# Kernel optimization log

Hardware: AMD Instinct MI355X
Metric: run time of the kernel (lower is better)

Reference implementation:

```python
import jax, jax.numpy as jnp
import numpy as np
from jax import lax

NG = 2   # n_groups
NH = 4   # n_heads
LN_EPS = 1e-5

SOBEL_X = np.array([[-1., 0., 1.], [-2., 0., 2.], [-1., 0., 1.]], np.float32)
SOBEL_Y = np.array([[-1., -2., -1.], [0., 0., 0.], [1., 2., 1.]], np.float32)


def conv1x1(x, w, b=None):
    # x: (N, Ci, H, W), w: (Co, Ci)
    y = jnp.einsum('oi,bihw->bohw', w, x)
    if b is not None:
        y = y + b[None, :, None, None]
    return y


def dwconv3(x, w, b=None):
    # depthwise 3x3, stride 1, padding 1. w: (C, 1, 3, 3)
    y = lax.conv_general_dilated(x, w, (1, 1), ((1, 1), (1, 1)),
                                 feature_group_count=x.shape[1],
                                 dimension_numbers=('NCHW', 'OIHW', 'NCHW'))
    if b is not None:
        y = y + b[None, :, None, None]
    return y


def grid_sample_bilinear(img, grid):
    # img: (N, C, H, W); grid: (N, Hg, Wg, 2) with (x, y) in [-1, 1]
    # align_corners=True, zero padding (matches F.grid_sample defaults used here)
    N, C, H, W = img.shape
    gx = (grid[..., 0] + 1.0) * 0.5 * (W - 1)
    gy = (grid[..., 1] + 1.0) * 0.5 * (H - 1)
    x0 = jnp.floor(gx)
    y0 = jnp.floor(gy)
    wx1 = gx - x0
    wy1 = gy - y0

    def gather(yy, xx):
        valid = (yy >= 0) & (yy < H) & (xx >= 0) & (xx < W)
        yc = jnp.clip(yy, 0, H - 1).astype(jnp.int32)
        xc = jnp.clip(xx, 0, W - 1).astype(jnp.int32)
        vals = jax.vmap(lambda im, y_, x_: im[:, y_, x_])(img, yc, xc)  # (N,C,Hg,Wg)
        return vals * valid[:, None, :, :].astype(img.dtype)

    v00 = gather(y0, x0)
    v01 = gather(y0, x0 + 1)
    v10 = gather(y0 + 1, x0)
    v11 = gather(y0 + 1, x0 + 1)
    w00 = ((1 - wy1) * (1 - wx1))[:, None]
    w01 = ((1 - wy1) * wx1)[:, None]
    w10 = (wy1 * (1 - wx1))[:, None]
    w11 = (wy1 * wx1)[:, None]
    return v00 * w00 + v01 * w01 + v10 * w10 + v11 * w11


def setup_inputs() -> dict:
    key = jax.random.key(0)
    B, C, H, W = 4, 128, 48, 48
    Cg = C // NG
    ks = jax.random.split(key, 16)
    s = 0.02
    inp = {
        'x': jax.random.normal(ks[0], (B, C, H, W), jnp.float32),
        'qW': jax.random.normal(ks[1], (C, C), jnp.float32) * s,
        'qb': jnp.zeros((C,), jnp.float32),
        'kW': jax.random.normal(ks[2], (C, C), jnp.float32) * s,
        'kb': jnp.zeros((C,), jnp.float32),
        'vW': jax.random.normal(ks[3], (C, C), jnp.float32) * s,
        'vb': jnp.zeros((C,), jnp.float32),
        'oW': jax.random.normal(ks[4], (C, C), jnp.float32) * s,
        'ob': jnp.zeros((C,), jnp.float32),
        'off_dw_w': jax.random.normal(ks[5], (Cg, 1, 3, 3), jnp.float32) * 0.1,
        'off_dw_b': jnp.zeros((Cg,), jnp.float32),
        'ln_g': jnp.ones((Cg,), jnp.float32),
        'ln_b': jnp.zeros((Cg,), jnp.float32),
        'off_pw_w': jax.random.normal(ks[6], (2, Cg), jnp.float32) * s,
        'sob_w': jax.random.normal(ks[7], (1, Cg), jnp.float32) * 0.1,
        'sob_b': jnp.zeros((1,), jnp.float32),
        'rpe_w': jax.random.normal(ks[8], (C, 1, 3, 3), jnp.float32) * 0.1,
        'rpe_b': jnp.zeros((C,), jnp.float32),
    }
    return inp


def reference(x, qW, qb, kW, kb, vW, vb, oW, ob, off_dw_w, off_dw_b,
              ln_g, ln_b, off_pw_w, sob_w, sob_b, rpe_w, rpe_b):
    B, C, H, W = x.shape
    Cg = C // NG
    Dh = C // NH
    scale = Dh ** -0.5

    q = conv1x1(x, qW, qb)                                   # (B,C,H,W)
    q_off = q.reshape(B * NG, Cg, H, W)                      # (Bg,Cg,H,W)

    # offset branch: dwconv -> LayerNorm(channel) -> GELU -> 1x1 (no bias)
    t = dwconv3(q_off, off_dw_w, off_dw_b)
    tt = t.transpose(0, 2, 3, 1)                             # (Bg,H,W,Cg)
    mu = tt.mean(-1, keepdims=True)
    var = tt.var(-1, keepdims=True)
    tt = (tt - mu) / jnp.sqrt(var + LN_EPS) * ln_g + ln_b
    t = jax.nn.gelu(tt, approximate=False).transpose(0, 3, 1, 2)
    offset = conv1x1(t, off_pw_w)                            # (Bg,2,H,W)

    Hk, Wk = H, W
    n_sample = Hk * Wk
    off_range = jnp.array([1.0 / (Hk - 1.0), 1.0 / (Wk - 1.0)], x.dtype).reshape(1, 2, 1, 1)
    offset = jnp.tanh(offset) * off_range                    # offset_range_factor = 1
    offset = offset.transpose(0, 2, 3, 1)                    # (Bg,Hk,Wk,2)  (y,x)

    # reference points, normalized to [-1,1]
    ref_y = (jnp.linspace(0.5, Hk - 0.5, Hk, dtype=x.dtype) / (Hk - 1.0)) * 2.0 - 1.0
    ref_x = (jnp.linspace(0.5, Wk - 0.5, Wk, dtype=x.dtype) / (Wk - 1.0)) * 2.0 - 1.0
    ref = jnp.stack(jnp.meshgrid(ref_y, ref_x, indexing='ij'), axis=-1)  # (Hk,Wk,2)
    reference = jnp.broadcast_to(ref[None], (B * NG, Hk, Wk, 2))

    # Sobel gate on 1x1-projected q_off
    s = conv1x1(q_off, sob_w, sob_b)                         # (Bg,1,H,W)
    kx = jnp.asarray(SOBEL_X).reshape(1, 1, 3, 3)
    ky = jnp.asarray(SOBEL_Y).reshape(1, 1, 3, 3)
    gxm = dwconv3(s, kx)
    gym = dwconv3(s, ky)
    mag = jnp.sqrt(gxm ** 2 + gym ** 2)
    binary = (mag > 0.5).astype(x.dtype).transpose(0, 2, 3, 1)  # (Bg,H,W,1)

    pos = offset + reference * binary                        # (Bg,Hk,Wk,2) (y,x)

    xs = grid_sample_bilinear(x.reshape(B * NG, Cg, H, W), pos[..., ::-1])  # grid in (x,y)
    xs = xs.reshape(B, C, 1, n_sample)

    qf = q.reshape(B * NH, Dh, H * W)
    k = conv1x1(xs, kW, kb).reshape(B * NH, Dh, n_sample)
    v = conv1x1(xs, vW, vb).reshape(B * NH, Dh, n_sample)

    attn = jnp.einsum('bcm,bcn->bmn', qf, k) * scale         # (B*NH, HW, n_sample)
    lepe = dwconv3(q.reshape(B, C, H, W), rpe_w, rpe_b).reshape(B * NH, Dh, H * W)
    attn = jax.nn.softmax(attn, axis=2)                      # attn_drop: eval identity
    out = jnp.einsum('bmn,bcn->bcm', attn, v) + lepe
    out = out.reshape(B, C, H, W)
    y = conv1x1(out, oW, ob)                                 # proj_drop: eval identity
    return (y, pos, reference)
```

## Files before the change

### kernel.cpp

```cpp
#include <hip/hip_runtime.h>
#include <hip/hip_bf16.h>
#include <math.h>

#define B_   4
#define C_   128
#define H_   48
#define W_   48
#define HW_  2304
#define CG_  64
#define DH_  32
#define NZ_  6
#define SCALE_ 0.17677669529663687f
#define QS_    (0.17677669529663687f * 1.4426950408889634f)
#define INVQ_  (1.0f / QS_)

#define Y_OFF   0
#define POS_OFF 1179648
#define REF_OFF 1216512

#define OFF_XTBF  0
#define OFF_QBF   589824
#define OFF_KBF   1179648
#define OFF_VBF   1769472
#define OFF_XST   2359296
#define OFF_WBF   2949120
#define OFF_PRS   2981888
#define OFF_PROH  3203072
#define OFF_SMAPD 6742016
#define OFF_WEFF  6778880

typedef __attribute__((ext_vector_type(8))) short short8;
typedef __attribute__((ext_vector_type(4))) float f32x4;
typedef __attribute__((ext_vector_type(4))) _Float16 f16x4;
typedef __attribute__((ext_vector_type(8))) _Float16 f16x8;

__device__ inline unsigned short f2bf(float f) {
  unsigned u = __float_as_uint(f);
  u += 0x7fff + ((u >> 16) & 1);
  return (unsigned short)(u >> 16);
}
__device__ inline float bf2f(unsigned short s) {
  return __uint_as_float(((unsigned)s) << 16);
}

__device__ inline short8 pack8(const f32x4 a, const f32x4 b) {
  union { unsigned u[4]; short8 s; } r;
  asm("v_cvt_pk_bf16_f32 %0, %1, %2" : "=v"(r.u[0]) : "v"(a[0]), "v"(a[1]));
  asm("v_cvt_pk_bf16_f32 %0, %1, %2" : "=v"(r.u[1]) : "v"(a[2]), "v"(a[3]));
  asm("v_cvt_pk_bf16_f32 %0, %1, %2" : "=v"(r.u[2]) : "v"(b[0]), "v"(b[1]));
  asm("v_cvt_pk_bf16_f32 %0, %1, %2" : "=v"(r.u[3]) : "v"(b[2]), "v"(b[3]));
  return r.s;
}

__global__ __launch_bounds__(256) void k_pre(const float* __restrict__ x,
                                             const float* __restrict__ qW, const float* __restrict__ kW,
                                             const float* __restrict__ vW, const float* __restrict__ oW,
                                             const float* __restrict__ qb,
                                             const float* __restrict__ sob_w, const float* __restrict__ sob_b,
                                             unsigned short* __restrict__ xTbf,
                                             unsigned short* __restrict__ wbf,
                                             double* __restrict__ weff) {
  int bx = blockIdx.x;
  if (bx < 288) {
    __shared__ float tile[64][65];
    int p0 = (bx % 36) * 64, c0 = ((bx / 36) & 1) * 64, b = bx / 72;
    for (int idx = threadIdx.x; idx < 4096; idx += 256) {
      int cr = idx >> 6, pc = idx & 63;
      tile[cr][pc] = x[((size_t)(b * C_) + c0 + cr) * HW_ + p0 + pc];
    }
    __syncthreads();
    for (int idx = threadIdx.x; idx < 4096; idx += 256) {
      int pr = idx >> 6, cc = idx & 63;
      xTbf[((size_t)(b * HW_) + p0 + pr) * C_ + c0 + cc] = f2bf(tile[cc][pr]);
    }
  } else if (bx < 544) {
    int t = (bx - 288) * 256 + threadIdx.x;
    int which = t >> 14, i = t & 16383;
    const float* src = which == 0 ? qW : which == 1 ? kW : which == 2 ? vW : oW;
    wbf[t] = f2bf(src[i]);
  } else {
    int t = threadIdx.x;
    int g = t >> 7, i = t & 127;
    double acc = 0.0;
    for (int c = 0; c < 64; c++)
      acc += (double)sob_w[c] * (double)qW[(size_t)(g * 64 + c) * C_ + i];
    weff[t] = acc;
    if (t < 2) {
      double bb = (double)sob_b[0];
      for (int c = 0; c < 64; c++) bb += (double)sob_w[c] * (double)qb[t * 64 + c];
      weff[256 + t] = bb;
    }
  }
}

__global__ __launch_bounds__(256, 4) void k_qconv_smapd(const unsigned short* __restrict__ xTbf,
                                                        const unsigned short* __restrict__ wbf,
                                                        const float* __restrict__ qb,
                                                        const float* __restrict__ x,
                                                        const double* __restrict__ weff,
                                                        unsigned short* __restrict__ qbf,
                                                        double* __restrict__ smapd) {
  int bx = blockIdx.x;
  if (bx < 576) {
    int t = threadIdx.x, w = t >> 6, l = t & 63, lg = l >> 4, lo = l & 15;
    int m0 = (bx % 144) * 16, b = bx / 144, o0 = w * 32;
    const unsigned short* xrow = xTbf + ((size_t)(b * HW_) + m0 + lo) * C_ + lg * 8;
    f32x4 acc[2] = {{0.f,0.f,0.f,0.f},{0.f,0.f,0.f,0.f}};
#pragma unroll
    for (int kb = 0; kb < 4; kb++) {
      short8 xf = *(const short8*)(xrow + kb * 32);
#pragma unroll
      for (int os = 0; os < 2; os++) {
        short8 wf = *(const short8*)(wbf + (size_t)(o0 + os * 16 + lo) * C_ + kb * 32 + lg * 8);
        acc[os] = __builtin_amdgcn_mfma_f32_16x16x32_bf16(xf, wf, acc[os], 0, 0, 0);
      }
    }
#pragma unroll
    for (int os = 0; os < 2; os++) {
      int o = o0 + os * 16 + lo;
      float bi = qb[o];
#pragma unroll
      for (int r = 0; r < 4; r++) {
        int m = m0 + lg * 4 + r;
        qbf[((size_t)(b * HW_) + m) * C_ + o] = f2bf((acc[os][r] + bi) * QS_);
      }
    }
  } else {
    int bb = bx - 576;
    int p = (bb % 9) * 256 + threadIdx.x;
    int bg = bb / 9;
    int b = bg >> 1, g = bg & 1;
    const float* xb = x + (size_t)b * C_ * HW_ + p;
    const double* wv = weff + g * 128;
    double acc = weff[256 + g];
#pragma unroll 8
    for (int i = 0; i < 128; i++) acc += wv[i] * (double)xb[(size_t)i * HW_];
    smapd[bg * HW_ + p] = acc;
  }
}

__global__ __launch_bounds__(256) void k_offpos_sample(const unsigned short* __restrict__ qbf,
                                                       const double* __restrict__ s_map,
                                                       const float* __restrict__ dw_w,
                                                       const float* __restrict__ dw_b,
                                                       const float* __restrict__ ln_g,
                                                       const float* __restrict__ ln_b,
                                                       const float* __restrict__ pw_w,
                                                       const unsigned short* __restrict__ xTbf,
                                                       float* __restrict__ out,
                                                       unsigned short* __restrict__ xsT) {
  int widx = blockIdx.x * 4 + (threadIdx.x >> 6);
  int lane = threadIdx.x & 63;
  int bg = widx / HW_;
  int p = widx - bg * HW_;
  int h = p / W_, w = p - h * W_;
  int b = bg >> 1, g = bg & 1;
  const unsigned short* qc = qbf + (size_t)(b * HW_) * C_ + g * 64 + lane;
  float tv = dw_b[lane];
#pragma unroll
  for (int dy = -1; dy <= 1; dy++)
#pragma unroll
    for (int dx = -1; dx <= 1; dx++) {
      int hh = h + dy, ww = w + dx;
      if (hh >= 0 && hh < H_ && ww >= 0 && ww < W_) {
        float wgt = dw_w[lane * 9 + (dy + 1) * 3 + (dx + 1)] * INVQ_;
        tv += wgt * bf2f(qc[(size_t)(hh * W_ + ww) * C_]);
      }
    }
  float ssum = tv, ssq = tv * tv;
#pragma unroll
  for (int msk = 32; msk; msk >>= 1) {
    ssum += __shfl_xor(ssum, msk, 64);
    ssq  += __shfl_xor(ssq,  msk, 64);
  }
  float mu  = ssum * (1.0f / 64.0f);
  float var = ssq * (1.0f / 64.0f) - mu * mu;
  float uu  = (tv - mu) * rsqrtf(var + 1e-5f) * ln_g[lane] + ln_b[lane];
  float gl = 0.5f * uu * (1.0f + erff(uu * 0.70710678118654752f));
  float p0 = pw_w[lane] * gl, p1 = pw_w[64 + lane] * gl;
#pragma unroll
  for (int msk = 32; msk; msk >>= 1) {
    p0 += __shfl_xor(p0, msk, 64);
    p1 += __shfl_xor(p1, msk, 64);
  }
  const double sobx[9] = {-1., 0., 1., -2., 0., 2., -1., 0., 1.};
  const double soby[9] = {-1., -2., -1., 0., 0., 0., 1., 2., 1.};
  float off_y = tanhf(p0) * (1.0f / 47.0f);
  float off_x = tanhf(p1) * (1.0f / 47.0f);
  const double* sm = s_map + bg * HW_;
  double gx = 0., gy = 0.;
#pragma unroll
  for (int dy = -1; dy <= 1; dy++)
#pragma unroll
    for (int dx = -1; dx <= 1; dx++) {
      int hh = h + dy, ww = w + dx;
      if (hh >= 0 && hh < H_ && ww >= 0 && ww < W_) {
        double sv = sm[hh * W_ + ww];
        gx += sobx[(dy + 1) * 3 + dx + 1] * sv;
        gy += soby[(dy + 1) * 3 + dx + 1] * sv;
      }
    }
  double mag = sqrt(gx * gx + gy * gy);
  float bin = mag > 0.5 ? 1.0f : 0.0f;
  float ry = ((h + 0.5f) / 47.0f) * 2.0f - 1.0f;
  float rx = ((w + 0.5f) / 47.0f) * 2.0f - 1.0f;
  float py = off_y + ry * bin;
  float px = off_x + rx * bin;
  if (lane == 0) {
    int pi = (bg * HW_ + p) * 2;
    out[POS_OFF + pi]     = py;
    out[POS_OFF + pi + 1] = px;
    out[REF_OFF + pi]     = ry;
    out[REF_OFF + pi + 1] = rx;
  }
  float gxf = (px + 1.0f) * 0.5f * 47.0f;
  float gyf = (py + 1.0f) * 0.5f * 47.0f;
  float x0 = floorf(gxf), y0 = floorf(gyf);
  float wx1 = gxf - x0, wy1 = gyf - y0;
  float wx0 = 1.0f - wx1, wy0 = 1.0f - wy1;
  const unsigned short* base = xTbf + (size_t)(b * HW_) * C_ + g * 64 + lane;
  float acc = 0.0f;
#pragma unroll
  for (int cy = 0; cy < 2; cy++)
#pragma unroll
    for (int cx = 0; cx < 2; cx++) {
      float yy = y0 + (float)cy, xx = x0 + (float)cx;
      bool valid = (yy >= 0.f) && (yy < 48.f) && (xx >= 0.f) && (xx < 48.f);
      int yc = min(max((int)yy, 0), 47);
      int xc = min(max((int)xx, 0), 47);
      float wgt = (cy ? wy1 : wy0) * (cx ? wx1 : wx0);
      float vv = valid ? bf2f(base[(size_t)(yc * 48 + xc) * C_]) : 0.0f;
      acc += wgt * vv;
    }
  xsT[((size_t)(b * HW_) + p) * C_ + g * 64 + lane] = f2bf(acc);
}

__global__ __launch_bounds__(256, 4) void k_kvconv(const unsigned short* __restrict__ xsT,
                                                   const unsigned short* __restrict__ wbf,
                                                   const float* __restrict__ kbias,
                                                   const float* __restrict__ vbias,
                                                   unsigned short* __restrict__ kbf,
                                                   unsigned short* __restrict__ vbf) {
  int t = threadIdx.x, w = t >> 6, l = t & 63, lg = l >> 4, lo = l & 15;
  int n0 = blockIdx.x * 16, b = blockIdx.y, o0 = w * 32;
  const unsigned short* xrow = xsT + ((size_t)(b * HW_) + n0 + lo) * C_ + lg * 8;
  const unsigned short* wk = wbf + 16384;
  const unsigned short* wv = wbf + 32768;
  f32x4 ak[2] = {{0.f,0.f,0.f,0.f},{0.f,0.f,0.f,0.f}};
  f32x4 av[2] = {{0.f,0.f,0.f,0.f},{0.f,0.f,0.f,0.f}};
#pragma unroll
  for (int kb = 0; kb < 4; kb++) {
    short8 xf = *(const short8*)(xrow + kb * 32);
#pragma unroll
    for (int os = 0; os < 2; os++) {
      size_t wo = (size_t)(o0 + os * 16 + lo) * C_ + kb * 32 + lg * 8;
      short8 wkf = *(const short8*)(wk + wo);
      short8 wvf = *(const short8*)(wv + wo);
      ak[os] = __builtin_amdgcn_mfma_f32_16x16x32_bf16(xf, wkf, ak[os], 0, 0, 0);
      av[os] = __builtin_amdgcn_mfma_f32_16x16x32_bf16(wvf, xf, av[os], 0, 0, 0);
    }
  }
  int o32 = (n0 & 16) + lo;
  int vpos = (n0 & ~31) + ((o32 & 12) << 1) + (o32 & 3) + ((o32 >> 4) << 2);
#pragma unroll
  for (int os = 0; os < 2; os++) {
    int ok = o0 + os * 16 + lo;
    float bk_ = kbias[ok];
#pragma unroll
    for (int r = 0; r < 4; r++) {
      int n = n0 + lg * 4 + r;
      kbf[((size_t)(b * HW_) + n) * C_ + ok] = f2bf(ak[os][r] + bk_);
      int ov = o0 + os * 16 + lg * 4 + r;
      vbf[((size_t)(b * C_) + ov) * HW_ + vpos] = f2bf(av[os][r] + vbias[ov]);
    }
  }
}

#define EXPROW(SV, RS)                                                              \
  _Pragma("unroll")                                                                 \
  for (int r = 0; r < 4; r++) {                                                     \
    float e0, e1, e2, e3;                                                           \
    asm("v_exp_f32 %0, %1" : "=v"(e0) : "v"(SV##0[r]));                             \
    asm("v_exp_f32 %0, %1" : "=v"(e1) : "v"(SV##1[r]));                             \
    asm("v_exp_f32 %0, %1" : "=v"(e2) : "v"(SV##2[r]));                             \
    asm("v_exp_f32 %0, %1" : "=v"(e3) : "v"(SV##3[r]));                             \
    SV##0[r] = e0; SV##1[r] = e1; SV##2[r] = e2; SV##3[r] = e3;                     \
    RS += (e0 + e1) + (e2 + e3);                                                    \
  }

#define ATTN_BODY7(BK, BV, BKN, BVN, DOPREF)                                        \
  {                                                                                 \
    if (DOPREF) {                                                                   \
      _Pragma("unroll")                                                             \
      for (int sub = 0; sub < 4; sub++)                                             \
        BKN[sub] = *(const short8*)(kb_ + (size_t)(n0 + 64 + sub * 16 + lo) * C_);  \
      BVN[0] = *(const short8*)(vr0 + n0 + 64);                                     \
      BVN[1] = *(const short8*)(vr0 + n0 + 96);                                     \
      BVN[2] = *(const short8*)(vr1 + n0 + 64);                                     \
      BVN[3] = *(const short8*)(vr1 + n0 + 96);                                     \
    }                                                                               \
    f32x4 z = {0.f, 0.f, 0.f, 0.f};                                                 \
    __builtin_amdgcn_s_setprio(1);                                                  \
    f32x4 s0 = __builtin_amdgcn_mfma_f32_16x16x32_bf16(BK[0], aq0, z, 0, 0, 0);     \
    f32x4 s1 = __builtin_amdgcn_mfma_f32_16x16x32_bf16(BK[1], aq0, z, 0, 0, 0);     \
    f32x4 s2 = __builtin_amdgcn_mfma_f32_16x16x32_bf16(BK[2], aq0, z, 0, 0, 0);     \
    f32x4 s3 = __builtin_amdgcn_mfma_f32_16x16x32_bf16(BK[3], aq0, z, 0, 0, 0);     \
    __builtin_amdgcn_s_setprio(0);                                                  \
    EXPROW(s, rsum0)                                                                \
    short8 pa0 = pack8(s0, s1), pa1 = pack8(s2, s3);                                \
    __builtin_amdgcn_s_setprio(1);                                                  \
    f32x4 t0 = __builtin_amdgcn_mfma_f32_16x16x32_bf16(BK[0], aq1, z, 0, 0, 0);     \
    f32x4 t1 = __builtin_amdgcn_mfma_f32_16x16x32_bf16(BK[1], aq1, z, 0, 0, 0);     \
    f32x4 t2 = __builtin_amdgcn_mfma_f32_16x16x32_bf16(BK[2], aq1, z, 0, 0, 0);     \
    f32x4 t3 = __builtin_amdgcn_mfma_f32_16x16x32_bf16(BK[3], aq1, z, 0, 0, 0);     \
    acc00 = __builtin_amdgcn_mfma_f32_16x16x32_bf16(pa0, BV[0], acc00, 0, 0, 0);    \
    acc00 = __builtin_amdgcn_mfma_f32_16x16x32_bf16(pa1, BV[1], acc00, 0, 0, 0);    \
    acc01 = __builtin_amdgcn_mfma_f32_16x16x32_bf16(pa0, BV[2], acc01, 0, 0, 0);    \
    acc01 = __builtin_amdgcn_mfma_f32_16x16x32_bf16(pa1, BV[3], acc01, 0, 0, 0);    \
    __builtin_amdgcn_s_setprio(0);                                                  \
    EXPROW(t, rsum1)                                                                \
    short8 pb0 = pack8(t0, t1), pb1 = pack8(t2, t3);                                \
    __builtin_amdgcn_s_setprio(1);                                                  \
    acc10 = __builtin_amdgcn_mfma_f32_16x16x32_bf16(pb0, BV[0], acc10, 0, 0, 0);    \
    acc10 = __builtin_amdgcn_mfma_f32_16x16x32_bf16(pb1, BV[1], acc10, 0, 0, 0);    \
    acc11 = __builtin_amdgcn_mfma_f32_16x16x32_bf16(pb0, BV[2], acc11, 0, 0, 0);    \
    acc11 = __builtin_amdgcn_mfma_f32_16x16x32_bf16(pb1, BV[3], acc11, 0, 0, 0);    \
    __builtin_amdgcn_s_setprio(0);                                                  \
    n0 += 64;                                                                       \
  }

__global__ __launch_bounds__(256, 3) void k_attn7(const unsigned short* __restrict__ qbf,
                                                  const unsigned short* __restrict__ kbf,
                                                  const unsigned short* __restrict__ vpf,
                                                  _Float16* __restrict__ prOh,
                                                  float* __restrict__ prS) {
  int t = threadIdx.x, w = t >> 6, l = t & 63, lg = l >> 4, lo = l & 15;
  int bh = blockIdx.y, b = bh >> 2, hd = bh & 3, nz = blockIdx.z;
  int cb = hd * 32;
  int m0 = blockIdx.x * 128 + w * 32;
  const unsigned short* qrow = qbf + ((size_t)(b * HW_) + m0 + lo) * C_ + cb + lg * 8;
  short8 aq0 = *(const short8*)qrow;
  short8 aq1 = *(const short8*)(qrow + (size_t)16 * C_);
  const unsigned short* kb_ = kbf + (size_t)(b * HW_) * C_ + cb + lg * 8;
  const unsigned short* vr0 = vpf + (size_t)(b * C_ + cb + lo) * HW_ + lg * 8;
  const unsigned short* vr1 = vr0 + (size_t)16 * HW_;
  f32x4 acc00 = {0.f,0.f,0.f,0.f}, acc01 = {0.f,0.f,0.f,0.f};
  f32x4 acc10 = {0.f,0.f,0.f,0.f}, acc11 = {0.f,0.f,0.f,0.f};
  float rsum0 = 0.f, rsum1 = 0.f;
  int n0 = nz * 384;
  short8 bkA[4], bkB[4], bvA[4], bvB[4];
#pragma unroll
  for (int sub = 0; sub < 4; sub++)
    bkA[sub] = *(const short8*)(kb_ + (size_t)(n0 + sub * 16 + lo) * C_);
  bvA[0] = *(const short8*)(vr0 + n0);
  bvA[1] = *(const short8*)(vr0 + n0 + 32);
  bvA[2] = *(const short8*)(vr1 + n0);
  bvA[3] = *(const short8*)(vr1 + n0 + 32);
  for (int i3 = 0; i3 < 3; i3++) {
    ATTN_BODY7(bkA, bvA, bkB, bvB, true)
    ATTN_BODY7(bkB, bvB, bkA, bvA, (i3 < 2))
  }
  rsum0 += __shfl_xor(rsum0, 16, 64);
  rsum0 += __shfl_xor(rsum0, 32, 64);
  rsum1 += __shfl_xor(rsum1, 16, 64);
  rsum1 += __shfl_xor(rsum1, 32, 64);
  _Float16* pr = prOh + (size_t)nz * (B_ * HW_ * C_);
#pragma unroll
  for (int r = 0; r < 4; r++) {
    int m = m0 + lg * 4 + r;
    size_t oi = ((size_t)(b * HW_) + m) * C_ + cb;
    pr[oi + lo] = (_Float16)acc00[r];
    pr[oi + 16 + lo] = (_Float16)acc01[r];
    size_t oi2 = oi + (size_t)16 * C_;
    pr[oi2 + lo] = (_Float16)acc10[r];
    pr[oi2 + 16 + lo] = (_Float16)acc11[r];
  }
  if (l < 16) {
    prS[((size_t)(nz * 16) + bh) * HW_ + m0 + lo] = rsum0;
    prS[((size_t)(nz * 16) + bh) * HW_ + m0 + 16 + lo] = rsum1;
  }
}

__global__ __launch_bounds__(256) void k_out(const _Float16* __restrict__ prOh,
                                             const float* __restrict__ prS,
                                             const unsigned short* __restrict__ qbf,
                                             const float* __restrict__ rpe_w,
                                             const float* __restrict__ rpe_b,
                                             const unsigned short* __restrict__ wbf,
                                             const float* __restrict__ ob_,
                                             float* __restrict__ y) {
  __shared__ __align__(16) unsigned short lds[16][136];
  int t = threadIdx.x;
  int m0 = blockIdx.x * 16, b = blockIdx.y;
  {
    int mi = t >> 4, c8 = (t & 15) * 8;
    int m = m0 + mi;
    int hd = c8 >> 5;
    size_t oi = ((size_t)(b * HW_) + m) * C_ + c8;
    float rs = 0.f;
    float o[8] = {0.f,0.f,0.f,0.f,0.f,0.f,0.f,0.f};
#pragma unroll
    for (int nz = 0; nz < NZ_; nz++) {
      rs += prS[((size_t)(nz * 16) + b * 4 + hd) * HW_ + m];
      f16x8 v = *(const f16x8*)(prOh + (size_t)nz * (B_ * HW_ * C_) + oi);
#pragma unroll
      for (int j = 0; j < 8; j++) o[j] += (float)v[j];
    }
    float inv = 1.0f / rs;
    int h = m / W_, ww0 = m - h * W_;
    float lp[8];
#pragma unroll
    for (int j = 0; j < 8; j++) lp[j] = rpe_b[c8 + j];
#pragma unroll
    for (int dy = -1; dy <= 1; dy++)
#pragma unroll
      for (int dx = -1; dx <= 1; dx++) {
        int hh = h + dy, ww = ww0 + dx;
        if (hh >= 0 && hh < H_ && ww >= 0 && ww < W_) {
          int idx = (dy + 1) * 3 + (dx + 1);
          short8 q8 = *(const short8*)(qbf + ((size_t)(b * HW_) + hh * W_ + ww) * C_ + c8);
#pragma unroll
          for (int j = 0; j < 8; j++)
            lp[j] += rpe_w[(c8 + j) * 9 + idx] * INVQ_ * bf2f((unsigned short)q8[j]);
        }
      }
    short8 res;
#pragma unroll
    for (int j = 0; j < 8; j++) res[j] = (short)f2bf(o[j] * inv + lp[j]);
    *(short8*)&lds[mi][c8] = res;
  }
  __syncthreads();
  int w = t >> 6, l = t & 63, lg = l >> 4, lo = l & 15;
  int o0 = w * 32;
  const unsigned short* wo = wbf + 49152;
  f32x4 acc[2] = {{0.f,0.f,0.f,0.f},{0.f,0.f,0.f,0.f}};
#pragma unroll
  for (int kb = 0; kb < 4; kb++) {
    short8 xf = *(const short8*)&lds[lo][kb * 32 + lg * 8];
#pragma unroll
    for (int os = 0; os < 2; os++) {
      short8 wf = *(const short8*)(wo + (size_t)(o0 + os * 16 + lo) * C_ + kb * 32 + lg * 8);
      acc[os] = __builtin_amdgcn_mfma_f32_16x16x32_bf16(wf, xf, acc[os], 0, 0, 0);
    }
  }
#pragma unroll
  for (int os = 0; os < 2; os++)
#pragma unroll
    for (int r = 0; r < 4; r++) {
      int o = o0 + os * 16 + lg * 4 + r;
      y[((size_t)(b * C_) + o) * HW_ + m0 + lo] = acc[os][r] + ob_[o];
    }
}

extern "C" void kernel_launch(void* const* d_in, const int* in_sizes, int n_in,
                              void* d_out, int out_size, void* d_ws, size_t ws_size,
                              hipStream_t stream) {
  const float* x        = (const float*)d_in[0];
  const float* qW       = (const float*)d_in[1];
  const float* qb       = (const float*)d_in[2];
  const float* kW       = (const float*)d_in[3];
  const float* kb       = (const float*)d_in[4];
  const float* vW       = (const float*)d_in[5];
  const float* vb       = (const float*)d_in[6];
  const float* oW       = (const float*)d_in[7];
  const float* ob       = (const float*)d_in[8];
  const float* off_dw_w = (const float*)d_in[9];
  const float* off_dw_b = (const float*)d_in[10];
  const float* ln_g     = (const float*)d_in[11];
  const float* ln_b     = (const float*)d_in[12];
  const float* off_pw_w = (const float*)d_in[13];
  const float* sob_w    = (const float*)d_in[14];
  const float* sob_b    = (const float*)d_in[15];
  const float* rpe_w    = (const float*)d_in[16];
  const float* rpe_b    = (const float*)d_in[17];
  float* out = (float*)d_out;
  float* wsf = (float*)d_ws;
  unsigned short* xTbf  = (unsigned short*)(wsf + OFF_XTBF);
  unsigned short* qbf   = (unsigned short*)(wsf + OFF_QBF);
  unsigned short* kbf   = (unsigned short*)(wsf + OFF_KBF);
  unsigned short* vbf   = (unsigned short*)(wsf + OFF_VBF);
  unsigned short* xsT   = (unsigned short*)(wsf + OFF_XST);
  unsigned short* wbf   = (unsigned short*)(wsf + OFF_WBF);
  float* prS   = wsf + OFF_PRS;
  _Float16* prOh = (_Float16*)(wsf + OFF_PROH);
  double* smapd = (double*)(wsf + OFF_SMAPD);
  double* weff  = (double*)(wsf + OFF_WEFF);

  k_pre          <<<545,             256, 0, stream>>>(x, qW, kW, vW, oW, qb, sob_w, sob_b,
                                                       xTbf, wbf, weff);
  k_qconv_smapd  <<<648,             256, 0, stream>>>(xTbf, wbf, qb, x, weff, qbf, smapd);
  k_offpos_sample<<<4608,            256, 0, stream>>>(qbf, smapd, off_dw_w, off_dw_b,
                                                       ln_g, ln_b, off_pw_w, xTbf, out, xsT);
  k_kvconv       <<<dim3(144, 4),    256, 0, stream>>>(xsT, wbf, kb, vb, kbf, vbf);
  k_attn7        <<<dim3(18, 16, 6), 256, 0, stream>>>(qbf, kbf, vbf, prOh, prS);
  k_out          <<<dim3(144, 4),    256, 0, stream>>>(prOh, prS, qbf, rpe_w, rpe_b,
                                                       wbf, ob, out + Y_OFF);
}
```

Before: 134.7 us.

## Merge pre-processing and q-conv kernels, cut attention key splits to four

```diff
diff --git a/kernel.cpp b/kernel.cpp
--- a/kernel.cpp
+++ b/kernel.cpp
@@ -9,7 +9,7 @@
 #define HW_  2304
 #define CG_  64
 #define DH_  32
-#define NZ_  6
+#define NZ_  4
 #define SCALE_ 0.17677669529663687f
 #define QS_    (0.17677669529663687f * 1.4426950408889634f)
 #define INVQ_  (1.0f / QS_)
@@ -25,13 +25,11 @@
 #define OFF_XST   2359296
 #define OFF_WBF   2949120
 #define OFF_PRS   2981888
-#define OFF_PROH  3203072
-#define OFF_SMAPD 6742016
-#define OFF_WEFF  6778880
+#define OFF_PROH  4161536
+#define OFF_SMAPD 7184384
 
 typedef __attribute__((ext_vector_type(8))) short short8;
 typedef __attribute__((ext_vector_type(4))) float f32x4;
-typedef __attribute__((ext_vector_type(4))) _Float16 f16x4;
 typedef __attribute__((ext_vector_type(8))) _Float16 f16x8;
 
 __device__ inline unsigned short f2bf(float f) {
@@ -52,66 +50,56 @@
   return r.s;
 }
 
-__global__ __launch_bounds__(256) void k_pre(const float* __restrict__ x,
-                                             const float* __restrict__ qW, const float* __restrict__ kW,
-                                             const float* __restrict__ vW, const float* __restrict__ oW,
-                                             const float* __restrict__ qb,
-                                             const float* __restrict__ sob_w, const float* __restrict__ sob_b,
-                                             unsigned short* __restrict__ xTbf,
-                                             unsigned short* __restrict__ wbf,
-                                             double* __restrict__ weff) {
+__global__ __launch_bounds__(256) void k_front(const float* __restrict__ x,
+                                               const float* __restrict__ qW, const float* __restrict__ kW,
+                                               const float* __restrict__ vW, const float* __restrict__ oW,
+                                               const float* __restrict__ qb,
+                                               const float* __restrict__ sob_w, const float* __restrict__ sob_b,
+                                               unsigned short* __restrict__ xTbf,
+                                               unsigned short* __restrict__ wbf,
+                                               unsigned short* __restrict__ qbf,
+                                               double* __restrict__ smapd) {
+  __shared__ __align__(16) float tile[64][65];
   int bx = blockIdx.x;
+  int t = threadIdx.x;
   if (bx < 288) {
-    __shared__ float tile[64][65];
     int p0 = (bx % 36) * 64, c0 = ((bx / 36) & 1) * 64, b = bx / 72;
-    for (int idx = threadIdx.x; idx < 4096; idx += 256) {
+    for (int idx = t; idx < 4096; idx += 256) {
       int cr = idx >> 6, pc = idx & 63;
       tile[cr][pc] = x[((size_t)(b * C_) + c0 + cr) * HW_ + p0 + pc];
     }
     __syncthreads();
-    for (int idx = threadIdx.x; idx < 4096; idx += 256) {
+    for (int idx = t; idx < 4096; idx += 256) {
       int pr = idx >> 6, cc = idx & 63;
       xTbf[((size_t)(b * HW_) + p0 + pr) * C_ + c0 + cc] = f2bf(tile[cc][pr]);
     }
-  } else if (bx < 544) {
-    int t = (bx - 288) * 256 + threadIdx.x;
-    int which = t >> 14, i = t & 16383;
-    const float* src = which == 0 ? qW : which == 1 ? kW : which == 2 ? vW : oW;
-    wbf[t] = f2bf(src[i]);
-  } else {
-    int t = threadIdx.x;
-    int g = t >> 7, i = t & 127;
-    double acc = 0.0;
-    for (int c = 0; c < 64; c++)
-      acc += (double)sob_w[c] * (double)qW[(size_t)(g * 64 + c) * C_ + i];
-    weff[t] = acc;
-    if (t < 2) {
-      double bb = (double)sob_b[0];
-      for (int c = 0; c < 64; c++) bb += (double)sob_w[c] * (double)qb[t * 64 + c];
-      weff[256 + t] = bb;
-    }
-  }
-}
-
-__global__ __launch_bounds__(256, 4) void k_qconv_smapd(const unsigned short* __restrict__ xTbf,
-                                                        const unsigned short* __restrict__ wbf,
-                                                        const float* __restrict__ qb,
-                                                        const float* __restrict__ x,
-                                                        const double* __restrict__ weff,
-                                                        unsigned short* __restrict__ qbf,
-                                                        double* __restrict__ smapd) {
-  int bx = blockIdx.x;
-  if (bx < 576) {
-    int t = threadIdx.x, w = t >> 6, l = t & 63, lg = l >> 4, lo = l & 15;
-    int m0 = (bx % 144) * 16, b = bx / 144, o0 = w * 32;
-    const unsigned short* xrow = xTbf + ((size_t)(b * HW_) + m0 + lo) * C_ + lg * 8;
+  } else if (bx < 864) {
+    int bb = bx - 288;
+    int m0 = (bb % 144) * 16, b = bb / 144;
+    unsigned short (*xls)[136] = (unsigned short(*)[136])tile;
+#pragma unroll
+    for (int it = 0; it < 2; it++) {
+      int r = it * 64 + (t >> 2);
+      int quad = t & 3;
+      float4 v = *(const float4*)&x[((size_t)(b * C_) + r) * HW_ + m0 + quad * 4];
+      xls[quad * 4 + 0][r] = f2bf(v.x);
+      xls[quad * 4 + 1][r] = f2bf(v.y);
+      xls[quad * 4 + 2][r] = f2bf(v.z);
+      xls[quad * 4 + 3][r] = f2bf(v.w);
+    }
+    __syncthreads();
+    int w = t >> 6, l = t & 63, lg = l >> 4, lo = l & 15;
+    int o0 = w * 32;
     f32x4 acc[2] = {{0.f,0.f,0.f,0.f},{0.f,0.f,0.f,0.f}};
 #pragma unroll
     for (int kb = 0; kb < 4; kb++) {
-      short8 xf = *(const short8*)(xrow + kb * 32);
+      short8 xf = *(const short8*)&xls[lo][kb * 32 + lg * 8];
 #pragma unroll
       for (int os = 0; os < 2; os++) {
-        short8 wf = *(const short8*)(wbf + (size_t)(o0 + os * 16 + lo) * C_ + kb * 32 + lg * 8);
+        const float* wrow = qW + (size_t)(o0 + os * 16 + lo) * C_ + kb * 32 + lg * 8;
+        f32x4 wa = *(const f32x4*)wrow;
+        f32x4 wb = *(const f32x4*)(wrow + 4);
+        short8 wf = pack8(wa, wb);
         acc[os] = __builtin_amdgcn_mfma_f32_16x16x32_bf16(xf, wf, acc[os], 0, 0, 0);
       }
     }
@@ -125,17 +113,33 @@
         qbf[((size_t)(b * HW_) + m) * C_ + o] = f2bf((acc[os][r] + bi) * QS_);
       }
     }
+  } else if (bx < 936) {
+    int bb = bx - 864;
+    int bg = bb / 9, pgrp = bb % 9;
+    int b = bg >> 1, g = bg & 1;
+    __shared__ double wl[129];
+    if (t < 128) {
+      double a = 0.0;
+      for (int c = 0; c < 64; c++)
+        a += (double)sob_w[c] * (double)qW[(size_t)(g * 64 + c) * C_ + t];
+      wl[t] = a;
+    } else if (t == 128) {
+      double bb2 = (double)sob_b[0];
+      for (int c = 0; c < 64; c++) bb2 += (double)sob_w[c] * (double)qb[g * 64 + c];
+      wl[128] = bb2;
+    }
+    __syncthreads();
+    int p = pgrp * 256 + t;
+    const float* xb = x + (size_t)b * C_ * HW_ + p;
+    double acc = wl[128];
+#pragma unroll 8
+    for (int i = 0; i < 128; i++) acc += wl[i] * (double)xb[(size_t)i * HW_];
+    smapd[bg * HW_ + p] = acc;
   } else {
-    int bb = bx - 576;
-    int p = (bb % 9) * 256 + threadIdx.x;
-    int bg = bb / 9;
-    int b = bg >> 1, g = bg & 1;
-    const float* xb = x + (size_t)b * C_ * HW_ + p;
-    const double* wv = weff + g * 128;
-    double acc = weff[256 + g];
-#pragma unroll 8
-    for (int i = 0; i < 128; i++) acc += wv[i] * (double)xb[(size_t)i * HW_];
-    smapd[bg * HW_ + p] = acc;
+    int tt = (bx - 936) * 256 + t;
+    int which = tt >> 14, i = tt & 16383;
+    const float* src = which == 0 ? qW : which == 1 ? kW : which == 2 ? vW : oW;
+    wbf[tt] = f2bf(src[i]);
   }
 }
 
@@ -288,16 +292,16 @@
     RS += (e0 + e1) + (e2 + e3);                                                    \
   }
 
-#define ATTN_BODY7(BK, BV, BKN, BVN, DOPREF)                                        \
+#define ATTN_BODY5(BK, BKN, DOPREF)                                                 \
   {                                                                                 \
+    short8 bv0 = *(const short8*)(vr0 + n0);                                        \
+    short8 bv1 = *(const short8*)(vr0 + n0 + 32);                                   \
+    short8 bv2 = *(const short8*)(vr1 + n0);                                        \
+    short8 bv3 = *(const short8*)(vr1 + n0 + 32);                                   \
     if (DOPREF) {                                                                   \
       _Pragma("unroll")                                                             \
       for (int sub = 0; sub < 4; sub++)                                             \
         BKN[sub] = *(const short8*)(kb_ + (size_t)(n0 + 64 + sub * 16 + lo) * C_);  \
-      BVN[0] = *(const short8*)(vr0 + n0 + 64);                                     \
-      BVN[1] = *(const short8*)(vr0 + n0 + 96);                                     \
-      BVN[2] = *(const short8*)(vr1 + n0 + 64);                                     \
-      BVN[3] = *(const short8*)(vr1 + n0 + 96);                                     \
     }                                                                               \
     f32x4 z = {0.f, 0.f, 0.f, 0.f};                                                 \
     __builtin_amdgcn_s_setprio(1);                                                  \
@@ -313,23 +317,23 @@
     f32x4 t1 = __builtin_amdgcn_mfma_f32_16x16x32_bf16(BK[1], aq1, z, 0, 0, 0);     \
     f32x4 t2 = __builtin_amdgcn_mfma_f32_16x16x32_bf16(BK[2], aq1, z, 0, 0, 0);     \
     f32x4 t3 = __builtin_amdgcn_mfma_f32_16x16x32_bf16(BK[3], aq1, z, 0, 0, 0);     \
-    acc00 = __builtin_amdgcn_mfma_f32_16x16x32_bf16(pa0, BV[0], acc00, 0, 0, 0);    \
-    acc00 = __builtin_amdgcn_mfma_f32_16x16x32_bf16(pa1, BV[1], acc00, 0, 0, 0);    \
-    acc01 = __builtin_amdgcn_mfma_f32_16x16x32_bf16(pa0, BV[2], acc01, 0, 0, 0);    \
-    acc01 = __builtin_amdgcn_mfma_f32_16x16x32_bf16(pa1, BV[3], acc01, 0, 0, 0);    \
+    acc00 = __builtin_amdgcn_mfma_f32_16x16x32_bf16(pa0, bv0, acc00, 0, 0, 0);      \
+    acc00 = __builtin_amdgcn_mfma_f32_16x16x32_bf16(pa1, bv1, acc00, 0, 0, 0);      \
+    acc01 = __builtin_amdgcn_mfma_f32_16x16x32_bf16(pa0, bv2, acc01, 0, 0, 0);      \
+    acc01 = __builtin_amdgcn_mfma_f32_16x16x32_bf16(pa1, bv3, acc01, 0, 0, 0);      \
     __builtin_amdgcn_s_setprio(0);                                                  \
     EXPROW(t, rsum1)                                                                \
     short8 pb0 = pack8(t0, t1), pb1 = pack8(t2, t3);                                \
     __builtin_amdgcn_s_setprio(1);                                                  \
-    acc10 = __builtin_amdgcn_mfma_f32_16x16x32_bf16(pb0, BV[0], acc10, 0, 0, 0);    \
-    acc10 = __builtin_amdgcn_mfma_f32_16x16x32_bf16(pb1, BV[1], acc10, 0, 0, 0);    \
-    acc11 = __builtin_amdgcn_mfma_f32_16x16x32_bf16(pb0, BV[2], acc11, 0, 0, 0);    \
-    acc11 = __builtin_amdgcn_mfma_f32_16x16x32_bf16(pb1, BV[3], acc11, 0, 0, 0);    \
+    acc10 = __builtin_amdgcn_mfma_f32_16x16x32_bf16(pb0, bv0, acc10, 0, 0, 0);      \
+    acc10 = __builtin_amdgcn_mfma_f32_16x16x32_bf16(pb1, bv1, acc10, 0, 0, 0);      \
+    acc11 = __builtin_amdgcn_mfma_f32_16x16x32_bf16(pb0, bv2, acc11, 0, 0, 0);      \
+    acc11 = __builtin_amdgcn_mfma_f32_16x16x32_bf16(pb1, bv3, acc11, 0, 0, 0);      \
     __builtin_amdgcn_s_setprio(0);                                                  \
     n0 += 64;                                                                       \
   }
 
-__global__ __launch_bounds__(256, 3) void k_attn7(const unsigned short* __restrict__ qbf,
+__global__ __launch_bounds__(256, 3) void k_attn8(const unsigned short* __restrict__ qbf,
                                                   const unsigned short* __restrict__ kbf,
                                                   const unsigned short* __restrict__ vpf,
                                                   _Float16* __restrict__ prOh,
@@ -347,19 +351,16 @@
   f32x4 acc00 = {0.f,0.f,0.f,0.f}, acc01 = {0.f,0.f,0.f,0.f};
   f32x4 acc10 = {0.f,0.f,0.f,0.f}, acc11 = {0.f,0.f,0.f,0.f};
   float rsum0 = 0.f, rsum1 = 0.f;
-  int n0 = nz * 384;
-  short8 bkA[4], bkB[4], bvA[4], bvB[4];
+  int n0 = nz * 576;
+  short8 bkA[4], bkB[4];
 #pragma unroll
   for (int sub = 0; sub < 4; sub++)
     bkA[sub] = *(const short8*)(kb_ + (size_t)(n0 + sub * 16 + lo) * C_);
-  bvA[0] = *(const short8*)(vr0 + n0);
-  bvA[1] = *(const short8*)(vr0 + n0 + 32);
-  bvA[2] = *(const short8*)(vr1 + n0);
-  bvA[3] = *(const short8*)(vr1 + n0 + 32);
-  for (int i3 = 0; i3 < 3; i3++) {
-    ATTN_BODY7(bkA, bvA, bkB, bvB, true)
-    ATTN_BODY7(bkB, bvB, bkA, bvA, (i3 < 2))
-  }
+  for (int i4 = 0; i4 < 4; i4++) {
+    ATTN_BODY5(bkA, bkB, true)
+    ATTN_BODY5(bkB, bkA, (i4 < 3))
+  }
+  ATTN_BODY5(bkA, bkB, false)
   rsum0 += __shfl_xor(rsum0, 16, 64);
   rsum0 += __shfl_xor(rsum0, 32, 64);
   rsum1 += __shfl_xor(rsum1, 16, 64);
@@ -484,15 +485,13 @@
   float* prS   = wsf + OFF_PRS;
   _Float16* prOh = (_Float16*)(wsf + OFF_PROH);
   double* smapd = (double*)(wsf + OFF_SMAPD);
-  double* weff  = (double*)(wsf + OFF_WEFF);
-
-  k_pre          <<<545,             256, 0, stream>>>(x, qW, kW, vW, oW, qb, sob_w, sob_b,
-                                                       xTbf, wbf, weff);
-  k_qconv_smapd  <<<648,             256, 0, stream>>>(xTbf, wbf, qb, x, weff, qbf, smapd);
+
+  k_front        <<<1192,            256, 0, stream>>>(x, qW, kW, vW, oW, qb, sob_w, sob_b,
+                                                       xTbf, wbf, qbf, smapd);
   k_offpos_sample<<<4608,            256, 0, stream>>>(qbf, smapd, off_dw_w, off_dw_b,
                                                        ln_g, ln_b, off_pw_w, xTbf, out, xsT);
   k_kvconv       <<<dim3(144, 4),    256, 0, stream>>>(xsT, wbf, kb, vb, kbf, vbf);
-  k_attn7        <<<dim3(18, 16, 6), 256, 0, stream>>>(qbf, kbf, vbf, prOh, prS);
+  k_attn8        <<<dim3(18, 16, 4), 256, 0, stream>>>(qbf, kbf, vbf, prOh, prS);
   k_out          <<<dim3(144, 4),    256, 0, stream>>>(prOh, prS, qbf, rpe_w, rpe_b,
                                                        wbf, ob, out + Y_OFF);
 }
```

After: 130.6 us. -3.0%, faster.

## Reshape attention split: fewer key splits, smaller blocks, drop V prefetch

Applied to the files above, without the earlier changes.

```diff
diff --git a/kernel.cpp b/kernel.cpp
--- a/kernel.cpp
+++ b/kernel.cpp
@@ -9,7 +9,7 @@
 #define HW_  2304
 #define CG_  64
 #define DH_  32
-#define NZ_  6
+#define NZ_  4
 #define SCALE_ 0.17677669529663687f
 #define QS_    (0.17677669529663687f * 1.4426950408889634f)
 #define INVQ_  (1.0f / QS_)
@@ -25,13 +25,12 @@
 #define OFF_XST   2359296
 #define OFF_WBF   2949120
 #define OFF_PRS   2981888
-#define OFF_PROH  3203072
-#define OFF_SMAPD 6742016
-#define OFF_WEFF  6778880
+#define OFF_PROH  4161536
+#define OFF_SMAPD 7184384
+#define OFF_WEFF  7221248
 
 typedef __attribute__((ext_vector_type(8))) short short8;
 typedef __attribute__((ext_vector_type(4))) float f32x4;
-typedef __attribute__((ext_vector_type(4))) _Float16 f16x4;
 typedef __attribute__((ext_vector_type(8))) _Float16 f16x8;
 
 __device__ inline unsigned short f2bf(float f) {
@@ -288,16 +287,16 @@
     RS += (e0 + e1) + (e2 + e3);                                                    \
   }
 
-#define ATTN_BODY7(BK, BV, BKN, BVN, DOPREF)                                        \
+#define ATTN_BODY5(BK, BKN, DOPREF)                                                 \
   {                                                                                 \
+    short8 bv0 = *(const short8*)(vr0 + n0);                                        \
+    short8 bv1 = *(const short8*)(vr0 + n0 + 32);                                   \
+    short8 bv2 = *(const short8*)(vr1 + n0);                                        \
+    short8 bv3 = *(const short8*)(vr1 + n0 + 32);                                   \
     if (DOPREF) {                                                                   \
       _Pragma("unroll")                                                             \
       for (int sub = 0; sub < 4; sub++)                                             \
         BKN[sub] = *(const short8*)(kb_ + (size_t)(n0 + 64 + sub * 16 + lo) * C_);  \
-      BVN[0] = *(const short8*)(vr0 + n0 + 64);                                     \
-      BVN[1] = *(const short8*)(vr0 + n0 + 96);                                     \
-      BVN[2] = *(const short8*)(vr1 + n0 + 64);                                     \
-      BVN[3] = *(const short8*)(vr1 + n0 + 96);                                     \
     }                                                                               \
     f32x4 z = {0.f, 0.f, 0.f, 0.f};                                                 \
     __builtin_amdgcn_s_setprio(1);                                                  \
@@ -313,31 +312,31 @@
     f32x4 t1 = __builtin_amdgcn_mfma_f32_16x16x32_bf16(BK[1], aq1, z, 0, 0, 0);     \
     f32x4 t2 = __builtin_amdgcn_mfma_f32_16x16x32_bf16(BK[2], aq1, z, 0, 0, 0);     \
     f32x4 t3 = __builtin_amdgcn_mfma_f32_16x16x32_bf16(BK[3], aq1, z, 0, 0, 0);     \
-    acc00 = __builtin_amdgcn_mfma_f32_16x16x32_bf16(pa0, BV[0], acc00, 0, 0, 0);    \
-    acc00 = __builtin_amdgcn_mfma_f32_16x16x32_bf16(pa1, BV[1], acc00, 0, 0, 0);    \
-    acc01 = __builtin_amdgcn_mfma_f32_16x16x32_bf16(pa0, BV[2], acc01, 0, 0, 0);    \
-    acc01 = __builtin_amdgcn_mfma_f32_16x16x32_bf16(pa1, BV[3], acc01, 0, 0, 0);    \
+    acc00 = __builtin_amdgcn_mfma_f32_16x16x32_bf16(pa0, bv0, acc00, 0, 0, 0);      \
+    acc00 = __builtin_amdgcn_mfma_f32_16x16x32_bf16(pa1, bv1, acc00, 0, 0, 0);      \
+    acc01 = __builtin_amdgcn_mfma_f32_16x16x32_bf16(pa0, bv2, acc01, 0, 0, 0);      \
+    acc01 = __builtin_amdgcn_mfma_f32_16x16x32_bf16(pa1, bv3, acc01, 0, 0, 0);      \
     __builtin_amdgcn_s_setprio(0);                                                  \
     EXPROW(t, rsum1)                                                                \
     short8 pb0 = pack8(t0, t1), pb1 = pack8(t2, t3);                                \
     __builtin_amdgcn_s_setprio(1);                                                  \
-    acc10 = __builtin_amdgcn_mfma_f32_16x16x32_bf16(pb0, BV[0], acc10, 0, 0, 0);    \
-    acc10 = __builtin_amdgcn_mfma_f32_16x16x32_bf16(pb1, BV[1], acc10, 0, 0, 0);    \
-    acc11 = __builtin_amdgcn_mfma_f32_16x16x32_bf16(pb0, BV[2], acc11, 0, 0, 0);    \
-    acc11 = __builtin_amdgcn_mfma_f32_16x16x32_bf16(pb1, BV[3], acc11, 0, 0, 0);    \
+    acc10 = __builtin_amdgcn_mfma_f32_16x16x32_bf16(pb0, bv0, acc10, 0, 0, 0);      \
+    acc10 = __builtin_amdgcn_mfma_f32_16x16x32_bf16(pb1, bv1, acc10, 0, 0, 0);      \
+    acc11 = __builtin_amdgcn_mfma_f32_16x16x32_bf16(pb0, bv2, acc11, 0, 0, 0);      \
+    acc11 = __builtin_amdgcn_mfma_f32_16x16x32_bf16(pb1, bv3, acc11, 0, 0, 0);      \
     __builtin_amdgcn_s_setprio(0);                                                  \
     n0 += 64;                                                                       \
   }
 
-__global__ __launch_bounds__(256, 3) void k_attn7(const unsigned short* __restrict__ qbf,
-                                                  const unsigned short* __restrict__ kbf,
-                                                  const unsigned short* __restrict__ vpf,
-                                                  _Float16* __restrict__ prOh,
-                                                  float* __restrict__ prS) {
+__global__ __launch_bounds__(128) void k_attn9(const unsigned short* __restrict__ qbf,
+                                               const unsigned short* __restrict__ kbf,
+                                               const unsigned short* __restrict__ vpf,
+                                               _Float16* __restrict__ prOh,
+                                               float* __restrict__ prS) {
   int t = threadIdx.x, w = t >> 6, l = t & 63, lg = l >> 4, lo = l & 15;
   int bh = blockIdx.y, b = bh >> 2, hd = bh & 3, nz = blockIdx.z;
   int cb = hd * 32;
-  int m0 = blockIdx.x * 128 + w * 32;
+  int m0 = blockIdx.x * 64 + w * 32;
   const unsigned short* qrow = qbf + ((size_t)(b * HW_) + m0 + lo) * C_ + cb + lg * 8;
   short8 aq0 = *(const short8*)qrow;
   short8 aq1 = *(const short8*)(qrow + (size_t)16 * C_);
@@ -347,19 +346,16 @@
   f32x4 acc00 = {0.f,0.f,0.f,0.f}, acc01 = {0.f,0.f,0.f,0.f};
   f32x4 acc10 = {0.f,0.f,0.f,0.f}, acc11 = {0.f,0.f,0.f,0.f};
   float rsum0 = 0.f, rsum1 = 0.f;
-  int n0 = nz * 384;
-  short8 bkA[4], bkB[4], bvA[4], bvB[4];
+  int n0 = nz * 576;
+  short8 bkA[4], bkB[4];
 #pragma unroll
   for (int sub = 0; sub < 4; sub++)
     bkA[sub] = *(const short8*)(kb_ + (size_t)(n0 + sub * 16 + lo) * C_);
-  bvA[0] = *(const short8*)(vr0 + n0);
-  bvA[1] = *(const short8*)(vr0 + n0 + 32);
-  bvA[2] = *(const short8*)(vr1 + n0);
-  bvA[3] = *(const short8*)(vr1 + n0 + 32);
-  for (int i3 = 0; i3 < 3; i3++) {
-    ATTN_BODY7(bkA, bvA, bkB, bvB, true)
-    ATTN_BODY7(bkB, bvB, bkA, bvA, (i3 < 2))
-  }
+  for (int i4 = 0; i4 < 4; i4++) {
+    ATTN_BODY5(bkA, bkB, true)
+    ATTN_BODY5(bkB, bkA, (i4 < 3))
+  }
+  ATTN_BODY5(bkA, bkB, false)
   rsum0 += __shfl_xor(rsum0, 16, 64);
   rsum0 += __shfl_xor(rsum0, 32, 64);
   rsum1 += __shfl_xor(rsum1, 16, 64);
@@ -492,7 +488,7 @@
   k_offpos_sample<<<4608,            256, 0, stream>>>(qbf, smapd, off_dw_w, off_dw_b,
                                                        ln_g, ln_b, off_pw_w, xTbf, out, xsT);
   k_kvconv       <<<dim3(144, 4),    256, 0, stream>>>(xsT, wbf, kb, vb, kbf, vbf);
-  k_attn7        <<<dim3(18, 16, 6), 256, 0, stream>>>(qbf, kbf, vbf, prOh, prS);
+  k_attn9        <<<dim3(36, 16, 4), 128, 0, stream>>>(qbf, kbf, vbf, prOh, prS);
   k_out          <<<dim3(144, 4),    256, 0, stream>>>(prOh, prS, qbf, rpe_w, rpe_b,
                                                        wbf, ob, out + Y_OFF);
 }
```

New measurement: 134.3 us. About the same (-0.3%).
